# Performance work log

Hardware: AMD Instinct MI355X
Metric: run time of the kernel (lower is better)

Reference implementation:

```python
import jax, jax.numpy as jnp
import numpy as np

B, L, DIM = 4, 2048, 512
H, D = 8, 64
SCALE = D ** -0.5
NEG = -10000.0


def setup_inputs() -> dict:
    key = jax.random.key(0)
    ks = jax.random.split(key, 5)
    std = 1.0 / np.sqrt(DIM)
    return {
        "x": jax.random.normal(ks[0], (B, L, DIM), dtype=jnp.float32),
        "wq": jax.random.normal(ks[1], (H * D, DIM), dtype=jnp.float32) * std,
        "wk": jax.random.normal(ks[2], (H * D, DIM), dtype=jnp.float32) * std,
        "wv": jax.random.normal(ks[3], (H * D, DIM), dtype=jnp.float32) * std,
        "wo": jax.random.normal(ks[4], (DIM, H * D), dtype=jnp.float32) * std,
    }


def reference(x, wq, wk, wv, wo):
    b, l, _ = x.shape
    # projections (torch Linear: y = x @ W.T), split heads -> [b,h,l,d]
    q = (x @ wq.T).reshape(b, l, H, D).transpose(0, 2, 1, 3)
    k = (x @ wk.T).reshape(b, l, H, D).transpose(0, 2, 1, 3)
    v = (x @ wv.T).reshape(b, l, H, D).transpose(0, 2, 1, 3)
    scores = jnp.einsum("bhld,bhsd->bhls", q, k) * SCALE
    scores = jnp.nan_to_num(scores, nan=0.0, posinf=10000.0, neginf=NEG)
    diag = jnp.eye(l, dtype=bool)[None, None]  # [1,1,l,l]
    scores = jnp.where(diag, NEG, scores)
    attn = jax.nn.softmax(scores, axis=-1)
    attn = jnp.where(diag, 0.0, attn)
    attn = jnp.nan_to_num(attn, nan=0.0, posinf=0.0, neginf=0.0)
    out = jnp.einsum("bhls,bhsd->bhld", attn, v)
    out = out.transpose(0, 2, 1, 3).reshape(b, l, H * D)
    return out @ wo.T
```

## Files before the change

### kernel.cpp

```cpp
#include <hip/hip_runtime.h>
#include <hip/hip_bf16.h>


#define Bsz 4
#define Lsz 2048
#define DIMsz 512
#define Hsz 8
#define Dsz 64

typedef _Float16 f16;
typedef __attribute__((ext_vector_type(8))) _Float16 f16x8;
typedef __attribute__((ext_vector_type(4))) _Float16 f16x4;
typedef __attribute__((ext_vector_type(2))) __fp16 fp16x2;
typedef __attribute__((ext_vector_type(4))) float f32x4;
typedef __attribute__((ext_vector_type(16))) float f32x16;
typedef unsigned int u32;
typedef __attribute__((ext_vector_type(2))) unsigned int u32x2;

#if __has_builtin(__builtin_amdgcn_exp2f)
#define EXP2(x) __builtin_amdgcn_exp2f(x)
#else
#define EXP2(x) __expf(0.6931471805599453f * (x))
#endif

__device__ __forceinline__ u32 pack2(float a, float b) {
#if __has_builtin(__builtin_amdgcn_cvt_pkrtz)
    fp16x2 h = __builtin_amdgcn_cvt_pkrtz(a, b);
    return __builtin_bit_cast(u32, h);
#else
    fp16x2 h; h.x = (__fp16)a; h.y = (__fp16)b;
    return __builtin_bit_cast(u32, h);
#endif
}

#if __has_builtin(__builtin_amdgcn_permlane32_swap)
__device__ __forceinline__ void plswap(u32& a, u32& b) {
    u32x2 r = __builtin_amdgcn_permlane32_swap(a, b, false, false);
    a = r.x; b = r.y;
}
#else
__device__ __forceinline__ void plswap(u32& a, u32& b) {
    u32 sa = (u32)__shfl_xor((int)a, 32);
    u32 sb = (u32)__shfl_xor((int)b, 32);
    bool hi = (threadIdx.x & 32) != 0;
    u32 na = hi ? sb : a;
    u32 nb = hi ? b : sa;
    a = na; b = nb;
}
#endif

__device__ __forceinline__ void gl2lds16(const void* g, void* l) {
    __builtin_amdgcn_global_load_lds(
        (const __attribute__((address_space(1))) u32*)g,
        (__attribute__((address_space(3))) u32*)l, 16, 0, 0);
}

__global__ __launch_bounds__(256) void pack_f16(
    const float* __restrict__ x, const float* __restrict__ wq,
    const float* __restrict__ wk, const float* __restrict__ wv,
    const float* __restrict__ wo,
    f16* __restrict__ xh, f16* __restrict__ w3h, f16* __restrict__ woh)
{
    int bx = blockIdx.x, seg, blk;
    if (bx < 4096) { seg = 0; blk = bx; }
    else { seg = 1 + ((bx - 4096) >> 8); blk = (bx - 4096) & 255; }
    const float* s; f16* d; float sc = 1.0f;
    switch (seg) {
        case 0: s = x;  d = xh;            break;
        case 1: s = wq; d = w3h;           sc = 0.18033688011112042f; break;
        case 2: s = wk; d = w3h + 262144;  break;
        case 3: s = wv; d = w3h + 524288;  break;
        default: s = wo; d = woh;          break;
    }
    int i = (blk * 256 + threadIdx.x) * 4;
    float4 v = *(const float4*)(s + i);
    f16x4 o;
    o.x = (f16)(v.x * sc); o.y = (f16)(v.y * sc);
    o.z = (f16)(v.z * sc); o.w = (f16)(v.w * sc);
    *(f16x4*)(d + i) = o;
}

__global__ __launch_bounds__(256) void gemm_qkv_f16(
    const f16* __restrict__ A, const f16* __restrict__ B,
    f16* __restrict__ qh, f16* __restrict__ kh, f16* __restrict__ vth)
{
    __shared__ __align__(16) char smem[32768];
    f16* Ash = (f16*)smem;
    f16* Bsh = (f16*)(smem + 16384);

    const int tid = threadIdx.x;
    const int w = tid >> 6, lane = tid & 63;
    const int quad = lane >> 4, low = lane & 15;
    const int wm = w >> 1, wn = w & 1;
    const int m0 = blockIdx.y * 128, n0 = blockIdx.x * 128;

    f32x4 acc[4][4];
    #pragma unroll
    for (int i = 0; i < 4; i++)
        #pragma unroll
        for (int j = 0; j < 4; j++) acc[i][j] = (f32x4){0.f, 0.f, 0.f, 0.f};

    #pragma unroll 1
    for (int k0 = 0; k0 < DIMsz; k0 += 64) {
        __syncthreads();
        #pragma unroll
        for (int j = 0; j < 4; j++) {
            int t = j * 256 + tid;
            int r = t >> 3, g = t & 7;
            int gc = (g ^ (r & 7)) * 8;
            char* lb = (char*)Ash + (j * 256 + w * 64) * 16;
            gl2lds16(A + (size_t)(m0 + r) * DIMsz + k0 + gc, lb);
            char* lb2 = (char*)Bsh + (j * 256 + w * 64) * 16;
            gl2lds16(B + (size_t)(n0 + r) * DIMsz + k0 + gc, lb2);
        }
        __syncthreads();

        #pragma unroll
        for (int ks2 = 0; ks2 < 2; ks2++) {
            f16x8 af[4], bf[4];
            #pragma unroll
            for (int mt = 0; mt < 4; mt++) {
                int ar = wm * 64 + mt * 16 + low;
                int c = ks2 * 4 + quad;
                af[mt] = *(const f16x8*)&Ash[ar * 64 + ((c ^ (ar & 7)) << 3)];
            }
            #pragma unroll
            for (int nt = 0; nt < 4; nt++) {
                int br = wn * 64 + nt * 16 + low;
                int c = ks2 * 4 + quad;
                bf[nt] = *(const f16x8*)&Bsh[br * 64 + ((c ^ (br & 7)) << 3)];
            }
            #pragma unroll
            for (int mt = 0; mt < 4; mt++)
                #pragma unroll
                for (int nt = 0; nt < 4; nt++)
                    acc[mt][nt] = __builtin_amdgcn_mfma_f32_16x16x32_f16(
                        af[mt], bf[nt], acc[mt][nt], 0, 0, 0);
        }
    }

    const int proj = n0 >> 9;
    if (proj < 2) {
        f16* dst = (proj == 0) ? qh : kh;
        #pragma unroll
        for (int nt = 0; nt < 4; nt++) {
            int n = n0 + wn * 64 + nt * 16 + low;
            int c = n & 511, h = c >> 6, d = c & 63;
            #pragma unroll
            for (int mt = 0; mt < 4; mt++)
                #pragma unroll
                for (int r = 0; r < 4; r++) {
                    int m = m0 + wm * 64 + mt * 16 + quad * 4 + r;
                    int b_ = m >> 11, l = m & (Lsz - 1);
                    size_t bh = (size_t)(b_ * Hsz + h);
                    dst[(bh * Lsz + l) * Dsz + d] = (f16)acc[mt][nt][r];
                }
        }
    } else {
        const int hb = (n0 & 511) >> 6;
        f16* Tv = (f16*)smem;
        const int b_ = m0 >> 11, l0 = m0 & (Lsz - 1);
        #pragma unroll 1
        for (int hs = 0; hs < 2; hs++) {
            __syncthreads();
            if (wn == hs) {
                #pragma unroll
                for (int nt = 0; nt < 4; nt++) {
                    int d = nt * 16 + low;
                    #pragma unroll
                    for (int mt = 0; mt < 4; mt++)
                        #pragma unroll
                        for (int r = 0; r < 4; r++) {
                            int l = wm * 64 + mt * 16 + quad * 4 + r;
                            Tv[d * 136 + l] = (f16)acc[mt][nt][r];
                        }
                }
            }
            __syncthreads();
            int d = tid >> 2, seg = tid & 3;
            size_t bh = (size_t)(b_ * Hsz + hb + hs);
            f16* dstp = vth + (bh * 64 + d) * (size_t)Lsz + l0 + seg * 32;
            const f16* srcp = Tv + d * 136 + seg * 32;
            #pragma unroll
            for (int j = 0; j < 4; j++)
                *(f16x8*)(dstp + j * 8) = *(const f16x8*)(srcp + j * 8);
        }
    }
}

__global__ __launch_bounds__(256, 2) void attn_mfma(
    const f16* __restrict__ q, const f16* __restrict__ k,
    const f16* __restrict__ vt, f16* __restrict__ ctx)
{
    __shared__ __align__(16) char smem[65536];

    const int tid = threadIdx.x;
    const int w = tid >> 6, lane = tid & 63;
    const int col = lane & 31;
    const int h = lane >> 5;
    const int bh = blockIdx.x;
    const int qb = blockIdx.y;
    const int q0 = qb * 64;
    const size_t kvb = (size_t)bh * Lsz;

    f16* Ks = (f16*)smem;
    f16* Vs = (f16*)(smem + 16384);

    f16x8 qf[2][4];
    #pragma unroll
    for (int qt = 0; qt < 2; qt++)
        #pragma unroll
        for (int s = 0; s < 4; s++)
            qf[qt][s] = *(const f16x8*)(q + (kvb + q0 + qt * 32 + col) * Dsz
                                          + s * 16 + h * 8);
    #pragma unroll
    for (int qt = 0; qt < 2; qt++)
        #pragma unroll
        for (int s = 0; s < 4; s++)
            asm volatile("" :: "v"(qf[qt][s]));

    const f16* kp; const f16* vp;
    {
        int rk_ = tid >> 3, gk = tid & 7;
        kp = k + (kvb + rk_) * Dsz + ((gk ^ (rk_ & 7)) << 3);
        int rv = tid >> 4, gv = tid & 15;
        vp = vt + ((size_t)bh * Dsz + rv) * Lsz + ((gv ^ (rv & 15)) << 3);
    }
    char* kl = (char*)smem + w * 1024;
    char* vl = (char*)smem + 16384 + w * 1024;

    const int rk = w * 32 + col;
    const f16* kfp[4];
    #pragma unroll
    for (int s = 0; s < 4; s++)
        kfp[s] = Ks + rk * 64 + (((s * 2 + h) ^ (rk & 7)) << 3);
    const f16* vfp[2][2];
    #pragma unroll
    for (int dt = 0; dt < 2; dt++)
        #pragma unroll
        for (int ks = 0; ks < 2; ks++) {
            int rv = dt * 32 + col, cv = w * 4 + ks * 2 + h;
            vfp[dt][ks] = Vs + rv * 128 + ((cv ^ (rv & 15)) << 3);
        }

    f32x16 acc[2][2];
    #pragma unroll
    for (int qt = 0; qt < 2; qt++)
        #pragma unroll
        for (int dt = 0; dt < 2; dt++)
            #pragma unroll
            for (int i = 0; i < 16; i++) acc[qt][dt][i] = 0.f;
    float lsum[2] = {0.f, 0.f};

    const int drd_s0 = (qb >> 1) * 128;
    const int dqt = w - (qb & 1) * 2;

    gl2lds16(kp,        kl);
    gl2lds16(kp + 2048, kl + 4096);
    gl2lds16(kp + 4096, kl + 8192);
    gl2lds16(kp + 6144, kl + 12288);
    gl2lds16(vp,            vl);
    gl2lds16(vp + 16 * Lsz, vl + 4096);
    gl2lds16(vp + 32 * Lsz, vl + 8192);
    gl2lds16(vp + 48 * Lsz, vl + 12288);
    kp += 128 * Dsz;
    vp += 128;

#define ATTN_ROUND(S0, P, PRE) do {                                           \
    const int bufoff_ = (P) * 32768;                                          \
    if (PRE) {                                                                \
        const int nx_ = ((P) ^ 1) * 32768;                                    \
        gl2lds16(kp,        kl + nx_);                                        \
        gl2lds16(kp + 2048, kl + nx_ + 4096);                                 \
        gl2lds16(kp + 4096, kl + nx_ + 8192);                                 \
        gl2lds16(kp + 6144, kl + nx_ + 12288);                                \
        gl2lds16(vp,            vl + nx_);                                    \
        gl2lds16(vp + 16 * Lsz, vl + nx_ + 4096);                             \
        gl2lds16(vp + 32 * Lsz, vl + nx_ + 8192);                             \
        gl2lds16(vp + 48 * Lsz, vl + nx_ + 12288);                            \
        kp += 128 * Dsz;                                                      \
        vp += 128;                                                            \
        asm volatile("s_waitcnt vmcnt(8)" ::: "memory");                      \
    } else {                                                                  \
        asm volatile("s_waitcnt vmcnt(0)" ::: "memory");                      \
    }                                                                         \
    __builtin_amdgcn_s_barrier();                                             \
    __builtin_amdgcn_sched_barrier(0);                                        \
    \
    f32x16 st[2];                                                             \
    _Pragma("unroll")                                                         \
    for (int i = 0; i < 16; i++) { st[0][i] = 0.f; st[1][i] = 0.f; }          \
    __builtin_amdgcn_s_setprio(1);                                            \
    _Pragma("unroll")                                                         \
    for (int s = 0; s < 4; s++) {                                             \
        f16x8 kf = *(const f16x8*)((const char*)kfp[s] + bufoff_);            \
        st[0] = __builtin_amdgcn_mfma_f32_32x32x16_f16(kf, qf[0][s],          \
                                                       st[0], 0, 0, 0);       \
        st[1] = __builtin_amdgcn_mfma_f32_32x32x16_f16(kf, qf[1][s],          \
                                                       st[1], 0, 0, 0);       \
    }                                                                         \
    __builtin_amdgcn_s_setprio(0);                                            \
                \
    union { u32 u[4]; f16x8 v; } pf[2][2];                                    \
    const bool drnd_ = ((S0) == drd_s0);                                      \
    _Pragma("unroll")                                                         \
    for (int qt = 0; qt < 2; qt++) {                                          \
        float pv[16];                                                         \
        _Pragma("unroll")                                                     \
        for (int i = 0; i < 16; i++) pv[i] = EXP2(st[qt][i]);                 \
        if (drnd_ && qt == dqt) {                                             \
            _Pragma("unroll")                                                 \
            for (int i = 0; i < 16; i++) {                                    \
                int row = (i & 3) + 8 * (i >> 2) + 4 * h;                     \
                pv[i] = (row == col) ? 0.f : pv[i];                           \
            }                                                                 \
        }                                                                     \
        _Pragma("unroll")                                                     \
        for (int i = 0; i < 16; i++) lsum[qt] += pv[i];                       \
        u32 P2[8];                                                            \
        _Pragma("unroll")                                                     \
        for (int j = 0; j < 8; j++)                                           \
            P2[j] = pack2(pv[2 * j], pv[2 * j + 1]);                          \
        plswap(P2[0], P2[2]); plswap(P2[1], P2[3]);                           \
        plswap(P2[4], P2[6]); plswap(P2[5], P2[7]);                           \
        _Pragma("unroll")                                                     \
        for (int jj = 0; jj < 4; jj++) {                                      \
            pf[qt][0].u[jj] = P2[jj];                                         \
            pf[qt][1].u[jj] = P2[4 + jj];                                     \
        }                                                                     \
    }                                                                         \
    \
    __builtin_amdgcn_s_setprio(1);                                            \
    _Pragma("unroll")                                                         \
    for (int dt = 0; dt < 2; dt++)                                            \
        _Pragma("unroll")                                                     \
        for (int ks = 0; ks < 2; ks++) {                                      \
            f16x8 vf = *(const f16x8*)((const char*)vfp[dt][ks] + bufoff_);   \
            acc[0][dt] = __builtin_amdgcn_mfma_f32_32x32x16_f16(              \
                vf, pf[0][ks].v, acc[0][dt], 0, 0, 0);                        \
            acc[1][dt] = __builtin_amdgcn_mfma_f32_32x32x16_f16(              \
                vf, pf[1][ks].v, acc[1][dt], 0, 0, 0);                        \
        }                                                                     \
    __builtin_amdgcn_s_setprio(0);                                            \
    __builtin_amdgcn_sched_barrier(0);                                        \
    __builtin_amdgcn_s_barrier();                                             \
} while (0)

    #pragma unroll 1
    for (int s0 = 0; s0 < Lsz; s0 += 256) {
        ATTN_ROUND(s0, 0, true);
        ATTN_ROUND(s0 + 128, 1, (s0 + 256 < Lsz));
    }
#undef ATTN_ROUND

    float* Lsp = (float*)(smem + 49152);
    #pragma unroll
    for (int qt = 0; qt < 2; qt++) {
        lsum[qt] += __shfl_xor(lsum[qt], 32);
        if (h == 0) Lsp[w * 64 + qt * 32 + col] = lsum[qt];
    }

    float* Om = (float*)smem;
    __syncthreads();
    if (w == 1 || w == 3) {
        float* og = Om + (w >> 1) * 4096;
        #pragma unroll
        for (int qt = 0; qt < 2; qt++)
            #pragma unroll
            for (int dt = 0; dt < 2; dt++)
                #pragma unroll
                for (int i = 0; i < 16; i++) {
                    int row = (i & 3) + 8 * (i >> 2) + 4 * h;
                    og[(dt * 32 + row) * 64 + qt * 32 + col] = acc[qt][dt][i];
                }
    }
    __syncthreads();
    if (w == 0 || w == 2) {
        const float* og = Om + (w >> 1) * 4096;
        #pragma unroll
        for (int qt = 0; qt < 2; qt++)
            #pragma unroll
            for (int dt = 0; dt < 2; dt++)
                #pragma unroll
                for (int i = 0; i < 16; i++) {
                    int row = (i & 3) + 8 * (i >> 2) + 4 * h;
                    acc[qt][dt][i] += og[(dt * 32 + row) * 64 + qt * 32 + col];
                }
    }
    __syncthreads();
    if (w == 2) {
        #pragma unroll
        for (int qt = 0; qt < 2; qt++)
            #pragma unroll
            for (int dt = 0; dt < 2; dt++)
                #pragma unroll
                for (int i = 0; i < 16; i++) {
                    int row = (i & 3) + 8 * (i >> 2) + 4 * h;
                    Om[(dt * 32 + row) * 64 + qt * 32 + col] = acc[qt][dt][i];
                }
    }
    __syncthreads();
    if (w == 0) {
        #pragma unroll
        for (int qt = 0; qt < 2; qt++)
            #pragma unroll
            for (int dt = 0; dt < 2; dt++)
                #pragma unroll
                for (int i = 0; i < 16; i++) {
                    int row = (i & 3) + 8 * (i >> 2) + 4 * h;
                    acc[qt][dt][i] += Om[(dt * 32 + row) * 64 + qt * 32 + col];
                }
        const int b = bh >> 3, hh = bh & 7;
        #pragma unroll
        for (int qt = 0; qt < 2; qt++) {
            float ls = Lsp[qt * 32 + col] + Lsp[64 + qt * 32 + col]
                     + Lsp[128 + qt * 32 + col] + Lsp[192 + qt * 32 + col];
            const float inv = 1.0f / ls;
            f16* op = ctx + ((size_t)(b * Lsz + q0 + qt * 32 + col)) * DIMsz
                          + hh * 64;
            #pragma unroll
            for (int dt = 0; dt < 2; dt++)
                #pragma unroll
                for (int r4 = 0; r4 < 4; r4++) {
                    f16x4 o;
                    o.x = (f16)(acc[qt][dt][4 * r4 + 0] * inv);
                    o.y = (f16)(acc[qt][dt][4 * r4 + 1] * inv);
                    o.z = (f16)(acc[qt][dt][4 * r4 + 2] * inv);
                    o.w = (f16)(acc[qt][dt][4 * r4 + 3] * inv);
                    *(f16x4*)(op + dt * 32 + 8 * r4 + 4 * h) = o;
                }
        }
    }
}

__global__ __launch_bounds__(256) void gemm_out_f16(
    const f16* __restrict__ A, const f16* __restrict__ B,
    float* __restrict__ C)
{
    __shared__ f16 Ash[64 * 64];
    __shared__ f16 Bsh[64 * 64];
    const int tid = threadIdx.x;
    const int w = tid >> 6, lane = tid & 63;
    const int quad = lane >> 4, low = lane & 15;
    const int wm = w >> 1, wn = w & 1;
    const int m0 = blockIdx.y * 64, n0 = blockIdx.x * 64;

    f32x4 acc[2][2];
    #pragma unroll
    for (int i = 0; i < 2; i++)
        #pragma unroll
        for (int j = 0; j < 2; j++) acc[i][j] = (f32x4){0.f, 0.f, 0.f, 0.f};

    #pragma unroll 1
    for (int k0 = 0; k0 < DIMsz; k0 += 64) {
        __syncthreads();
        #pragma unroll
        for (int j = 0; j < 2; j++) {
            int t = j * 256 + tid;
            int r = t >> 3, g = t & 7;
            int gc = (g ^ (r & 7)) * 8;
            char* lb = (char*)Ash + (j * 256 + w * 64) * 16;
            gl2lds16(A + (size_t)(m0 + r) * DIMsz + k0 + gc, lb);
            char* lb2 = (char*)Bsh + (j * 256 + w * 64) * 16;
            gl2lds16(B + (size_t)(n0 + r) * DIMsz + k0 + gc, lb2);
        }
        __syncthreads();

        #pragma unroll
        for (int ks2 = 0; ks2 < 2; ks2++) {
            f16x8 af[2], bf[2];
            #pragma unroll
            for (int mt = 0; mt < 2; mt++) {
                int ar = wm * 32 + mt * 16 + low;
                int c = ks2 * 4 + quad;
                af[mt] = *(const f16x8*)&Ash[ar * 64 + ((c ^ (ar & 7)) << 3)];
            }
            #pragma unroll
            for (int nt = 0; nt < 2; nt++) {
                int br = wn * 32 + nt * 16 + low;
                int c = ks2 * 4 + quad;
                bf[nt] = *(const f16x8*)&Bsh[br * 64 + ((c ^ (br & 7)) << 3)];
            }
            #pragma unroll
            for (int mt = 0; mt < 2; mt++)
                #pragma unroll
                for (int nt = 0; nt < 2; nt++)
                    acc[mt][nt] = __builtin_amdgcn_mfma_f32_16x16x32_f16(
                        af[mt], bf[nt], acc[mt][nt], 0, 0, 0);
        }
    }

    #pragma unroll
    for (int mt = 0; mt < 2; mt++)
        #pragma unroll
        for (int r = 0; r < 4; r++) {
            int m = m0 + wm * 32 + mt * 16 + quad * 4 + r;
            #pragma unroll
            for (int nt = 0; nt < 2; nt++) {
                int n = n0 + wn * 32 + nt * 16 + low;
                C[(size_t)m * DIMsz + n] = acc[mt][nt][r];
            }
        }
}

extern "C" void kernel_launch(void* const* d_in, const int* in_sizes, int n_in,
                              void* d_out, int out_size, void* d_ws, size_t ws_size,
                              hipStream_t stream) {
    const float* x  = (const float*)d_in[0];
    const float* wq = (const float*)d_in[1];
    const float* wk = (const float*)d_in[2];
    const float* wv = (const float*)d_in[3];
    const float* wo = (const float*)d_in[4];
    float* out = (float*)d_out;

    const size_t NTOK = (size_t)Bsz * Lsz;
    const size_t XSZ  = NTOK * DIMsz;

    f16* xh   = (f16*)d_ws;
    f16* w3h  = xh + XSZ;
    f16* woh  = w3h + 3 * 262144;
    f16* qh   = woh + 262144;
    f16* kh   = qh + XSZ;
    f16* vth  = kh + XSZ;
    f16* ctxh = vth + XSZ;

    pack_f16<<<5120, 256, 0, stream>>>(x, wq, wk, wv, wo, xh, w3h, woh);

    dim3 g1(1536 / 128, NTOK / 128);
    gemm_qkv_f16<<<g1, 256, 0, stream>>>(xh, w3h, qh, kh, vth);

    dim3 g2(Bsz * Hsz, Lsz / 64);
    attn_mfma<<<g2, 256, 0, stream>>>(qh, kh, vth, ctxh);

    dim3 g3(DIMsz / 64, NTOK / 64);
    gemm_out_f16<<<g3, 256, 0, stream>>>(ctxh, woh, out);
}
```

Before: 165.2 us.

## Single-buffer K tile in LDS to fit three attention blocks per CU

Shrinks the attention kernel's LDS from 64KB to 48KB by keeping only one K buffer. V stays double-buffered. Each round now loads the K fragments into registers, waits, and synchronises before issuing the next K prefetch into the same buffer. Launch bounds are raised to allow three blocks per CU, trading an extra barrier, an lgkm wait and more register pressure per round for higher occupancy.

```diff
diff --git a/kernel.cpp b/kernel.cpp
--- a/kernel.cpp
+++ b/kernel.cpp
@@ -188,11 +188,11 @@
     }
 }
 
-__global__ __launch_bounds__(256, 2) void attn_mfma(
+__global__ __launch_bounds__(256, 3) void attn_mfma(
     const f16* __restrict__ q, const f16* __restrict__ k,
     const f16* __restrict__ vt, f16* __restrict__ ctx)
 {
-    __shared__ __align__(16) char smem[65536];
+    __shared__ __align__(16) char smem[49152];
 
     const int tid = threadIdx.x;
     const int w = tid >> 6, lane = tid & 63;
@@ -259,33 +259,41 @@
     gl2lds16(kp + 2048, kl + 4096);
     gl2lds16(kp + 4096, kl + 8192);
     gl2lds16(kp + 6144, kl + 12288);
+    kp += 128 * Dsz;
     gl2lds16(vp,            vl);
     gl2lds16(vp + 16 * Lsz, vl + 4096);
     gl2lds16(vp + 32 * Lsz, vl + 8192);
     gl2lds16(vp + 48 * Lsz, vl + 12288);
-    kp += 128 * Dsz;
     vp += 128;
 
 #define ATTN_ROUND(S0, P, PRE) do {                                           \
-    const int bufoff_ = (P) * 32768;                                          \
     if (PRE) {                                                                \
-        const int nx_ = ((P) ^ 1) * 32768;                                    \
-        gl2lds16(kp,        kl + nx_);                                        \
-        gl2lds16(kp + 2048, kl + nx_ + 4096);                                 \
-        gl2lds16(kp + 4096, kl + nx_ + 8192);                                 \
-        gl2lds16(kp + 6144, kl + nx_ + 12288);                                \
-        gl2lds16(vp,            vl + nx_);                                    \
-        gl2lds16(vp + 16 * Lsz, vl + nx_ + 4096);                             \
-        gl2lds16(vp + 32 * Lsz, vl + nx_ + 8192);                             \
-        gl2lds16(vp + 48 * Lsz, vl + nx_ + 12288);                            \
-        kp += 128 * Dsz;                                                      \
+        const int nv_ = ((P) ^ 1) * 16384;                                    \
+        gl2lds16(vp,            vl + nv_);                                    \
+        gl2lds16(vp + 16 * Lsz, vl + nv_ + 4096);                             \
+        gl2lds16(vp + 32 * Lsz, vl + nv_ + 8192);                             \
+        gl2lds16(vp + 48 * Lsz, vl + nv_ + 12288);                            \
         vp += 128;                                                            \
-        asm volatile("s_waitcnt vmcnt(8)" ::: "memory");                      \
+        asm volatile("s_waitcnt vmcnt(4)" ::: "memory");                      \
     } else {                                                                  \
         asm volatile("s_waitcnt vmcnt(0)" ::: "memory");                      \
     }                                                                         \
     __builtin_amdgcn_s_barrier();                                             \
     __builtin_amdgcn_sched_barrier(0);                                        \
+        \
+    f16x8 kf_[4];                                                             \
+    _Pragma("unroll")                                                         \
+    for (int s = 0; s < 4; s++) kf_[s] = *(const f16x8*)kfp[s];               \
+    asm volatile("s_waitcnt lgkmcnt(0)" ::: "memory");                        \
+    __builtin_amdgcn_sched_barrier(0);                                        \
+    __builtin_amdgcn_s_barrier();                                             \
+    if (PRE) {                                                                \
+        gl2lds16(kp,        kl);                                              \
+        gl2lds16(kp + 2048, kl + 4096);                                       \
+        gl2lds16(kp + 4096, kl + 8192);                                       \
+        gl2lds16(kp + 6144, kl + 12288);                                      \
+        kp += 128 * Dsz;                                                      \
+    }                                                                         \
     \
     f32x16 st[2];                                                             \
     _Pragma("unroll")                                                         \
@@ -293,10 +301,9 @@
     __builtin_amdgcn_s_setprio(1);                                            \
     _Pragma("unroll")                                                         \
     for (int s = 0; s < 4; s++) {                                             \
-        f16x8 kf = *(const f16x8*)((const char*)kfp[s] + bufoff_);            \
-        st[0] = __builtin_amdgcn_mfma_f32_32x32x16_f16(kf, qf[0][s],          \
+        st[0] = __builtin_amdgcn_mfma_f32_32x32x16_f16(kf_[s], qf[0][s],      \
                                                        st[0], 0, 0, 0);       \
-        st[1] = __builtin_amdgcn_mfma_f32_32x32x16_f16(kf, qf[1][s],          \
+        st[1] = __builtin_amdgcn_mfma_f32_32x32x16_f16(kf_[s], qf[1][s],      \
                                                        st[1], 0, 0, 0);       \
     }                                                                         \
     __builtin_amdgcn_s_setprio(0);                                            \
@@ -335,7 +342,8 @@
     for (int dt = 0; dt < 2; dt++)                                            \
         _Pragma("unroll")                                                     \
         for (int ks = 0; ks < 2; ks++) {                                      \
-            f16x8 vf = *(const f16x8*)((const char*)vfp[dt][ks] + bufoff_);   \
+            f16x8 vf = *(const f16x8*)((const char*)vfp[dt][ks]               \
+                                       + (P) * 16384);                        \
             acc[0][dt] = __builtin_amdgcn_mfma_f32_32x32x16_f16(              \
                 vf, pf[0][ks].v, acc[0][dt], 0, 0, 0);                        \
             acc[1][dt] = __builtin_amdgcn_mfma_f32_32x32x16_f16(              \
@@ -353,7 +361,9 @@
     }
 #undef ATTN_ROUND
 
-    float* Lsp = (float*)(smem + 49152);
+    __syncthreads();
+
+    float* Lsp = (float*)(smem + 32768);
     #pragma unroll
     for (int qt = 0; qt < 2; qt++) {
         lsum[qt] += __shfl_xor(lsum[qt], 32);
@@ -361,7 +371,6 @@
     }
 
     float* Om = (float*)smem;
-    __syncthreads();
     if (w == 1 || w == 3) {
         float* og = Om + (w >> 1) * 4096;
         #pragma unroll
```

Result: slower. 220.9 us (+33.7%).
